# Kernel tuning notes

Hardware: AMD Instinct MI355X
Metric: run time of the kernel (lower is better)

Reference implementation:

```python
import jax, jax.numpy as jnp
import numpy as np


def setup_inputs() -> dict:
    key = jax.random.key(0)
    k1, k2, k3 = jax.random.split(key, 3)
    B, C, D = 4096, 10000, 512
    feat = jax.random.normal(k1, (B, D), dtype=jnp.float32)
    label = jax.random.randint(k2, (B,), 0, C, dtype=jnp.int64)
    # xavier_uniform for weights [C, D]: bound = sqrt(6/(C+D))
    bound = np.sqrt(6.0 / (C + D)).astype(np.float32)
    weights = jax.random.uniform(k3, (C, D), dtype=jnp.float32, minval=-bound, maxval=bound)
    return {"feat": feat, "label": label, "weights": weights}


def reference(feat, label, weights):
    # pairwise squared L2 distance between feat [B,D] and weights [C,D]
    # computed via the Gram-matrix identity (same math as broadcast-sub-square-sum)
    f2 = jnp.sum(feat * feat, axis=-1, keepdims=True)          # [B,1]
    w2 = jnp.sum(weights * weights, axis=-1)[None, :]          # [1,C]
    cross = jnp.einsum('bd,cd->bc', feat, weights)             # [B,C]
    metric = jnp.maximum(f2 + w2 - 2.0 * cross, 0.0)           # [B,C] sq dists
    kernal_metric = jnp.exp(-0.01 * metric)                    # RBF kernel logits
    # original computes avg kernel value at true labels but then overrides
    # scale = 1.0, so logits are just the kernel values
    scale = 1.0
    train_logits = scale * kernal_metric
    valuation_logits = scale * kernal_metric
    return (train_logits, valuation_logits, weights)
```

## Files before the change

kernel.cpp:

```cpp
#include <hip/hip_runtime.h>
#include <hip/hip_bf16.h>
#include <stdint.h>

#define BDIM 4096
#define CDIM 10000
#define DDIM 512
#define CPAD 10112
#define NT 16

typedef __bf16 bf16_t;
typedef __attribute__((ext_vector_type(2))) __bf16 bf16x2;
typedef __attribute__((ext_vector_type(8))) __bf16 bf16x8;
typedef __attribute__((ext_vector_type(2))) float f32x2;
typedef __attribute__((ext_vector_type(4))) float f32x4;

__device__ __forceinline__ void gl_lds16(const void* g, void* s) {
  __builtin_amdgcn_global_load_lds(
      (const __attribute__((address_space(1))) void*)g,
      (__attribute__((address_space(3))) void*)s, 16, 0, 0);
}

__device__ __forceinline__ void lds_barrier() {
  asm volatile("s_waitcnt lgkmcnt(0)" ::: "memory");
  __builtin_amdgcn_s_barrier();
  __builtin_amdgcn_sched_barrier(0);
}

__global__ __launch_bounds__(256) void prep(
    const float* __restrict__ feat, const float* __restrict__ w,
    bf16_t* __restrict__ fb, bf16_t* __restrict__ wb,
    float* __restrict__ f2, float* __restrict__ w2,
    float* __restrict__ wout) {
  const int t = threadIdx.x;
  const int lane = t & 63;
  const int wv = t >> 6;
  const int r = blockIdx.x * 4 + wv;
  const int c0 = lane * 8;

  if (r < BDIM) {
    const f32x4 v0 = *(const f32x4*)(feat + (size_t)r * DDIM + c0);
    const f32x4 v1 = *(const f32x4*)(feat + (size_t)r * DDIM + c0 + 4);
    bf16x8 o;
#pragma unroll
    for (int j = 0; j < 4; ++j) {
      o[j] = (__bf16)v0[j];
      o[j + 4] = (__bf16)v1[j];
    }
    *(bf16x8*)(fb + (size_t)r * DDIM + c0) = o;
    float ss = v0.x * v0.x + v0.y * v0.y + v0.z * v0.z + v0.w * v0.w +
               v1.x * v1.x + v1.y * v1.y + v1.z * v1.z + v1.w * v1.w;
#pragma unroll
    for (int off = 32; off > 0; off >>= 1) ss += __shfl_down(ss, off);
    if (lane == 0) f2[r] = ss;
  } else {
    const int row = r - BDIM;
    if (row < CDIM) {
      const f32x4 v0 = *(const f32x4*)(w + (size_t)row * DDIM + c0);
      const f32x4 v1 = *(const f32x4*)(w + (size_t)row * DDIM + c0 + 4);
      __builtin_nontemporal_store(v0, (f32x4*)(wout + (size_t)row * DDIM + c0));
      __builtin_nontemporal_store(
          v1, (f32x4*)(wout + (size_t)row * DDIM + c0 + 4));
      bf16x8 o;
#pragma unroll
      for (int j = 0; j < 4; ++j) {
        o[j] = (__bf16)v0[j];
        o[j + 4] = (__bf16)v1[j];
      }
      *(bf16x8*)(wb + (size_t)row * DDIM + c0) = o;
      float ss = v0.x * v0.x + v0.y * v0.y + v0.z * v0.z + v0.w * v0.w +
                 v1.x * v1.x + v1.y * v1.y + v1.z * v1.z + v1.w * v1.w;
#pragma unroll
      for (int off = 32; off > 0; off >>= 1) ss += __shfl_down(ss, off);
      if (lane == 0) w2[row] = ss;
    } else if (row < CPAD) {
      bf16x8 z = {};
      *(bf16x8*)(wb + (size_t)row * DDIM + c0) = z;
      if (lane == 0) w2[row] = 0.0f;
    }
  }
}

__global__ __launch_bounds__(256, 4) void rbf_gemm(
    const bf16_t* __restrict__ A,
    const bf16_t* __restrict__ Bw,
    const float* __restrict__ f2g, const float* __restrict__ w2g,
    float* __restrict__ out) {
  __shared__ __align__(16) char pool[32768];
  bf16_t* Pb = (bf16_t*)pool;
  __shared__ float f2s[128];
  __shared__ float w2s[128];

  const int bid = blockIdx.x;
  const int wg = (bid & 7) * (2528 / 8) + (bid >> 3);
  const int bm = wg & 31;
  const int bn = wg >> 5;
  const int t = threadIdx.x;
  const int lane = t & 63;

  if (t < 128)
    f2s[t] = f2g[bm * 128 + t];
  else
    w2s[t - 128] = w2g[bn * 128 + (t - 128)];

  const int sr = t >> 2;
  const int sc = (t & 3) * 8;
  const bf16_t* ga0 = A + (size_t)(bm * 128 + sr) * DDIM + sc;
  const bf16_t* ga1 = ga0 + (size_t)64 * DDIM;
  const bf16_t* gb0 = Bw + (size_t)(bn * 128 + sr) * DDIM + sc;
  const bf16_t* gb1 = gb0 + (size_t)64 * DDIM;

  const int wv = t >> 6;
  const int wm = (wv >> 1) * 64;
  const int wn = (wv & 1) * 64;
  const int fr = lane & 15;
  const int k8 = (lane >> 4) * 8;
  const int g16 = lane >> 4;

#define STAGE(b, kt)                                \
  do {                                              \
    const int k0_ = (kt) * 32;                      \
    bf16_t* Ab_ = Pb + (b) * 8192;                  \
    gl_lds16(ga0 + k0_, Ab_ + t * 8);               \
    gl_lds16(ga1 + k0_, Ab_ + 2048 + t * 8);        \
    gl_lds16(gb0 + k0_, Ab_ + 4096 + t * 8);        \
    gl_lds16(gb1 + k0_, Ab_ + 4096 + 2048 + t * 8); \
  } while (0)

  f32x4 acc[4][4];
#pragma unroll
  for (int i = 0; i < 4; ++i)
#pragma unroll
    for (int j = 0; j < 4; ++j) acc[i][j] = (f32x4){0.f, 0.f, 0.f, 0.f};

  STAGE(0, 0);
  __syncthreads();

#pragma unroll
  for (int kt = 0; kt < NT; ++kt) {
    const int cur = kt & 1;
    if (kt + 1 < NT) STAGE(cur ^ 1, kt + 1);
    const bf16_t* Ab = Pb + cur * 8192;
    bf16x8 af[4], wf[4];
#pragma unroll
    for (int mi = 0; mi < 4; ++mi)
      af[mi] = *(const bf16x8*)(Ab + (wm + mi * 16 + fr) * 32 + k8);
#pragma unroll
    for (int ni = 0; ni < 4; ++ni)
      wf[ni] = *(const bf16x8*)(Ab + 4096 + (wn + ni * 16 + fr) * 32 + k8);
#pragma unroll
    for (int mi = 0; mi < 4; ++mi)
#pragma unroll
      for (int ni = 0; ni < 4; ++ni)
        acc[mi][ni] = __builtin_amdgcn_mfma_f32_16x16x32_bf16(
            wf[ni], af[mi], acc[mi][ni], 0, 0, 0);
    if (kt + 1 < NT) __syncthreads();
  }

  lds_barrier();

  float* slab = (float*)pool + wv * 2048;
  const size_t BC = (size_t)BDIM * CDIM;
  const int c_l = g16 * 4;

#pragma unroll
  for (int mi = 0; mi < 4; ++mi) {
    float* sb = slab + (mi & 1) * 1024;
    const float frow = f2s[wm + mi * 16 + fr];
#pragma unroll
    for (int ni = 0; ni < 4; ++ni) {
      const int cl = wn + ni * 16 + c_l;
      f32x4 st;
#pragma unroll
      for (int j = 0; j < 4; ++j) {
        float m = frow + w2s[cl + j] - 2.0f * acc[mi][ni][j];
        m = fmaxf(m, 0.0f);
        st[j] = __expf(-0.01f * m);
      }
      const int g = ni * 4 + g16;
      const int q = (g + fr) & 15;
      *(f32x4*)&sb[fr * 64 + q * 4] = st;
    }
#pragma unroll
    for (int s = 0; s < 4; ++s) {
      const int r = s * 4 + g16;
      const int g2 = lane & 15;
      const int q2 = (g2 + r) & 15;
      const f32x4 v = *(const f32x4*)&sb[r * 64 + q2 * 4];
      const int gcol = bn * 128 + wn + g2 * 4;
      if (gcol < CDIM) {
        float* p = out + (size_t)(bm * 128 + wm + mi * 16 + r) * CDIM + gcol;
        __builtin_nontemporal_store(v, (f32x4*)p);
        __builtin_nontemporal_store(v, (f32x4*)(p + BC));
      }
    }
  }
#undef STAGE
}

extern "C" void kernel_launch(void* const* d_in, const int* in_sizes, int n_in,
                              void* d_out, int out_size, void* d_ws,
                              size_t ws_size, hipStream_t stream) {
  const float* feat = (const float*)d_in[0];
  const float* w = (const float*)d_in[2];
  float* out = (float*)d_out;

  char* ws = (char*)d_ws;
  bf16_t* fb = (bf16_t*)ws;
  bf16_t* wb = (bf16_t*)(ws + 4194304);
  float* f2 = (float*)(ws + 4194304 + 10354688);
  float* w2 = (float*)(ws + 4194304 + 10354688 + 16384);

  float* wout = out + (size_t)2 * BDIM * CDIM;

  prep<<<(BDIM + CPAD) / 4, 256, 0, stream>>>(feat, w, fb, wb, f2, w2, wout);
  rbf_gemm<<<2528, 256, 0, stream>>>(fb, wb, f2, w2, out);
}
```

Measured before the change: 108.6 us.

## Prefetch A two stages ahead with triple buffering and partial vmcnt waits

```diff
diff --git a/kernel.cpp b/kernel.cpp
--- a/kernel.cpp
+++ b/kernel.cpp
@@ -85,10 +85,8 @@
     const bf16_t* __restrict__ Bw,
     const float* __restrict__ f2g, const float* __restrict__ w2g,
     float* __restrict__ out) {
-  __shared__ __align__(16) char pool[32768];
+  __shared__ __align__(16) char pool[40960];
   bf16_t* Pb = (bf16_t*)pool;
-  __shared__ float f2s[128];
-  __shared__ float w2s[128];
 
   const int bid = blockIdx.x;
   const int wg = (bid & 7) * (2528 / 8) + (bid >> 3);
@@ -97,10 +95,17 @@
   const int t = threadIdx.x;
   const int lane = t & 63;
 
-  if (t < 128)
-    f2s[t] = f2g[bm * 128 + t];
-  else
-    w2s[t - 128] = w2g[bn * 128 + (t - 128)];
+  const int wv = t >> 6;
+  const int wm = (wv >> 1) * 64;
+  const int wn = (wv & 1) * 64;
+  const int fr = lane & 15;
+  const int k8 = (lane >> 4) * 8;
+  const int g16 = lane >> 4;
+
+  float f2r[4];
+#pragma unroll
+  for (int mi = 0; mi < 4; ++mi)
+    f2r[mi] = f2g[bm * 128 + wm + mi * 16 + fr];
 
   const int sr = t >> 2;
   const int sc = (t & 3) * 8;
@@ -109,22 +114,18 @@
   const bf16_t* gb0 = Bw + (size_t)(bn * 128 + sr) * DDIM + sc;
   const bf16_t* gb1 = gb0 + (size_t)64 * DDIM;
 
-  const int wv = t >> 6;
-  const int wm = (wv >> 1) * 64;
-  const int wn = (wv & 1) * 64;
-  const int fr = lane & 15;
-  const int k8 = (lane >> 4) * 8;
-  const int g16 = lane >> 4;
-
-#define STAGE(b, kt)                                \
-  do {                                              \
-    const int k0_ = (kt) * 32;                      \
-    bf16_t* Ab_ = Pb + (b) * 8192;                  \
-    gl_lds16(ga0 + k0_, Ab_ + t * 8);               \
-    gl_lds16(ga1 + k0_, Ab_ + 2048 + t * 8);        \
-    gl_lds16(gb0 + k0_, Ab_ + 4096 + t * 8);        \
-    gl_lds16(gb1 + k0_, Ab_ + 4096 + 2048 + t * 8); \
+#define STAGE_A(buf, kt)                              \
+  do {                                                \
+    bf16_t* d_ = Pb + (buf) * 4096;                   \
+    gl_lds16(ga0 + (kt) * 32, d_ + t * 8);            \
+    gl_lds16(ga1 + (kt) * 32, d_ + 2048 + t * 8);     \
   } while (0)
+#define STAGE_B(buf, kt)                              \
+  do {                                                \
+    bf16_t* d_ = Pb + 12288 + (buf) * 4096;           \
+    gl_lds16(gb0 + (kt) * 32, d_ + t * 8);            \
+    gl_lds16(gb1 + (kt) * 32, d_ + 2048 + t * 8);     \
+  } while (0)
 
   f32x4 acc[4][4];
 #pragma unroll
@@ -132,28 +133,40 @@
 #pragma unroll
     for (int j = 0; j < 4; ++j) acc[i][j] = (f32x4){0.f, 0.f, 0.f, 0.f};
 
-  STAGE(0, 0);
-  __syncthreads();
+  STAGE_A(0, 0);
+  STAGE_B(0, 0);
+  STAGE_A(1, 1);
+  asm volatile("s_waitcnt vmcnt(2)" ::: "memory");
+  __builtin_amdgcn_s_barrier();
 
 #pragma unroll
   for (int kt = 0; kt < NT; ++kt) {
-    const int cur = kt & 1;
-    if (kt + 1 < NT) STAGE(cur ^ 1, kt + 1);
-    const bf16_t* Ab = Pb + cur * 8192;
+    if (kt + 1 < NT) STAGE_B((kt + 1) & 1, kt + 1);
+    if (kt + 2 < NT) STAGE_A((kt + 2) % 3, kt + 2);
+    const bf16_t* Abuf = Pb + (kt % 3) * 4096;
+    const bf16_t* Bbuf = Pb + 12288 + (kt & 1) * 4096;
     bf16x8 af[4], wf[4];
 #pragma unroll
     for (int mi = 0; mi < 4; ++mi)
-      af[mi] = *(const bf16x8*)(Ab + (wm + mi * 16 + fr) * 32 + k8);
+      af[mi] = *(const bf16x8*)(Abuf + (mi * 16 + fr + (wm >> 1) * 2) * 32 + k8);
 #pragma unroll
     for (int ni = 0; ni < 4; ++ni)
-      wf[ni] = *(const bf16x8*)(Ab + 4096 + (wn + ni * 16 + fr) * 32 + k8);
+      wf[ni] = *(const bf16x8*)(Bbuf + (wn + ni * 16 + fr) * 32 + k8);
+    __builtin_amdgcn_s_setprio(1);
 #pragma unroll
     for (int mi = 0; mi < 4; ++mi)
 #pragma unroll
       for (int ni = 0; ni < 4; ++ni)
         acc[mi][ni] = __builtin_amdgcn_mfma_f32_16x16x32_bf16(
             wf[ni], af[mi], acc[mi][ni], 0, 0, 0);
-    if (kt + 1 < NT) __syncthreads();
+    __builtin_amdgcn_s_setprio(0);
+    if (kt <= NT - 3) {
+      asm volatile("s_waitcnt vmcnt(2)" ::: "memory");
+      __builtin_amdgcn_s_barrier();
+    } else if (kt == NT - 2) {
+      asm volatile("s_waitcnt vmcnt(0)" ::: "memory");
+      __builtin_amdgcn_s_barrier();
+    }
   }
 
   lds_barrier();
@@ -162,17 +175,21 @@
   const size_t BC = (size_t)BDIM * CDIM;
   const int c_l = g16 * 4;
 
+  f32x4 w2v[4];
+#pragma unroll
+  for (int ni = 0; ni < 4; ++ni)
+    w2v[ni] = *(const f32x4*)(w2g + bn * 128 + wn + ni * 16 + c_l);
+
 #pragma unroll
   for (int mi = 0; mi < 4; ++mi) {
     float* sb = slab + (mi & 1) * 1024;
-    const float frow = f2s[wm + mi * 16 + fr];
+    const float frow = f2r[mi];
 #pragma unroll
     for (int ni = 0; ni < 4; ++ni) {
-      const int cl = wn + ni * 16 + c_l;
       f32x4 st;
 #pragma unroll
       for (int j = 0; j < 4; ++j) {
-        float m = frow + w2s[cl + j] - 2.0f * acc[mi][ni][j];
+        float m = frow + w2v[ni][j] - 2.0f * acc[mi][ni][j];
         m = fmaxf(m, 0.0f);
         st[j] = __expf(-0.01f * m);
       }
@@ -194,7 +211,8 @@
       }
     }
   }
-#undef STAGE
+#undef STAGE_A
+#undef STAGE_B
 }
 
 extern "C" void kernel_launch(void* const* d_in, const int* in_sizes, int n_in,
```

After: 108.2 us. About the same (-0.4%).
